# Kernel tuning notes

Measured on AMD Instinct MI355X. Metric: run time of the kernel, lower is better.

Reference implementation:

```python
import jax, jax.numpy as jnp
import numpy as np

N_NODES = 100000
N_EDGES = 640000
D_IN = 128
HIDDEN = 256
OUT = 256
NUM_GRAPHS = 256


def setup_inputs() -> dict:
    key = jax.random.key(0)
    ks = jax.random.split(key, 8)
    x = jax.random.normal(ks[0], (N_NODES, D_IN), dtype=jnp.float32)
    edge_index = jax.random.randint(ks[1], (2, N_EDGES), 0, N_NODES, dtype=jnp.int64)
    batch = jnp.sort(jax.random.randint(ks[2], (N_NODES,), 0, NUM_GRAPHS, dtype=jnp.int64))
    s1 = 1.0 / np.sqrt(D_IN)
    s2 = 1.0 / np.sqrt(HIDDEN)
    W1_l = jax.random.normal(ks[3], (D_IN, HIDDEN), dtype=jnp.float32) * s1
    W1_r = jax.random.normal(ks[4], (D_IN, HIDDEN), dtype=jnp.float32) * s1
    b1 = jnp.zeros((HIDDEN,), dtype=jnp.float32)
    W2_l = jax.random.normal(ks[5], (HIDDEN, OUT), dtype=jnp.float32) * s2
    W2_r = jax.random.normal(ks[6], (HIDDEN, OUT), dtype=jnp.float32) * s2
    b2 = jnp.zeros((OUT,), dtype=jnp.float32)
    return {"x": x, "edge_index": edge_index, "batch": batch,
            "W1_l": W1_l, "b1": b1, "W1_r": W1_r,
            "W2_l": W2_l, "b2": b2, "W2_r": W2_r}


def _sage_conv(x, src, dst, W_l, b_l, W_r):
    # PyG SAGEConv, aggr='mean': lin_l(mean_{j in N(i)} x_j) + lin_r(x_i)
    n = x.shape[0]
    msgs = x[src]                                              # [E, d] gather
    agg = jax.ops.segment_sum(msgs, dst, num_segments=n)       # [N, d] scatter-add
    cnt = jax.ops.segment_sum(jnp.ones((src.shape[0],), x.dtype), dst, num_segments=n)
    mean = agg / jnp.maximum(cnt, 1.0)[:, None]
    return mean @ W_l + b_l + x @ W_r


def reference(x, edge_index, batch, W1_l, b1, W1_r, W2_l, b2, W2_r):
    src, dst = edge_index[0], edge_index[1]
    h = jax.nn.relu(_sage_conv(x, src, dst, W1_l, b1, W1_r))
    h = _sage_conv(h, src, dst, W2_l, b2, W2_r)
    # global_add_pool: segment sum over per-node graph ids
    return jax.ops.segment_sum(h, batch, num_segments=NUM_GRAPHS)  # [G, OUT]
```

## Files before the change

kernel.cpp:

```cpp
#include <hip/hip_runtime.h>

#define NN 100000
#define NE 640000
#define DIN 128
#define DH 256
#define DOUT 256
#define NG 256
#define NB1 ((NN + 255) / 256)

#define PECH 157
#define CPE (4 * PECH)
#define PEB ((NE + CPE - 1) / CPE)
#define GSP 8

#define PNB 1024
#define CHN2 ((NN + PNB - 1) / PNB)

#define BCH 4096
#define BNB ((NE + BCH - 1) / BCH)

#define XCB (NN * DIN / 8 / 256)
#define CTB ((NE + 255) / 256)

typedef __bf16 bf16_t;
typedef __bf16 bf16x8 __attribute__((ext_vector_type(8)));
typedef __bf16 bf16x2 __attribute__((ext_vector_type(2)));
typedef float f32x4 __attribute__((ext_vector_type(4)));
typedef float f32v2 __attribute__((ext_vector_type(2)));

#if __has_builtin(__builtin_amdgcn_cvt_pk_fp8_f32) && __has_builtin(__builtin_amdgcn_cvt_pk_f32_fp8)
#define USE_HW_FP8 1
#else
#define USE_HW_FP8 0
#endif

#if !USE_HW_FP8
__device__ __forceinline__ unsigned f32_to_fp8_1(float f) {
  unsigned sg = (__float_as_uint(f) >> 31) << 7;
  float af = fabsf(f);
  unsigned body;
  if (af < 0.015625f) {
    body = (unsigned)(int)rintf(af * 512.0f);
  } else {
    unsigned bits = __float_as_uint(af);
    unsigned rb = bits + 0x7FFFFu + ((bits >> 20) & 1u);
    unsigned e = rb >> 23;
    body = ((e - 120u) << 3) | ((rb >> 20) & 7u);
  }
  return (sg | body) & 0xffu;
}
__device__ __forceinline__ float fp8_to_f32_1(unsigned b) {
  unsigned s = b >> 7, e = (b >> 3) & 15u, m = b & 7u;
  float v = (e == 0) ? (float)m * 0.001953125f
                     : __uint_as_float(((e + 120u) << 23) | (m << 20));
  return s ? -v : v;
}
#endif

__device__ __forceinline__ unsigned pack4_fp8(float v0, float v1, float v2, float v3) {
#if USE_HW_FP8
  int u = __builtin_amdgcn_cvt_pk_fp8_f32(v0, v1, 0, false);
  u = __builtin_amdgcn_cvt_pk_fp8_f32(v2, v3, u, true);
  return (unsigned)u;
#else
  return f32_to_fp8_1(v0) | (f32_to_fp8_1(v1) << 8) |
         (f32_to_fp8_1(v2) << 16) | (f32_to_fp8_1(v3) << 24);
#endif
}

__device__ __forceinline__ unsigned short pack2_fp8(float v0, float v1) {
#if USE_HW_FP8
  int u = __builtin_amdgcn_cvt_pk_fp8_f32(v0, v1, 0, false);
  return (unsigned short)(u & 0xffff);
#else
  return (unsigned short)(f32_to_fp8_1(v0) | (f32_to_fp8_1(v1) << 8));
#endif
}

__device__ __forceinline__ void unpack4_fp8(unsigned v, float* o) {
#if USE_HW_FP8
  f32v2 a = __builtin_amdgcn_cvt_pk_f32_fp8((int)v, false);
  f32v2 b = __builtin_amdgcn_cvt_pk_f32_fp8((int)v, true);
  o[0] = a[0]; o[1] = a[1]; o[2] = b[0]; o[3] = b[1];
#else
  o[0] = fp8_to_f32_1(v & 0xffu);         o[1] = fp8_to_f32_1((v >> 8) & 0xffu);
  o[2] = fp8_to_f32_1((v >> 16) & 0xffu); o[3] = fp8_to_f32_1(v >> 24);
#endif
}

__device__ __forceinline__ void unpack2_fp8(unsigned v, float* o) {
#if USE_HW_FP8
  f32v2 a = __builtin_amdgcn_cvt_pk_f32_fp8((int)v, false);
  o[0] = a[0]; o[1] = a[1];
#else
  o[0] = fp8_to_f32_1(v & 0xffu); o[1] = fp8_to_f32_1((v >> 8) & 0xffu);
#endif
}

__device__ __forceinline__ unsigned pack8_i4(const float* f) {
  unsigned nib = 0;
#pragma unroll
  for (int j = 0; j < 8; ++j) {
    int q = (int)rintf(f[j] * 2.0f);
    q = (q < -8) ? -8 : (q > 7 ? 7 : q);
    nib |= ((unsigned)(q & 15)) << (4 * j);
  }
  return nib;
}

__global__ void k_pre(const float* __restrict__ x, const int* __restrict__ dst,
                      const float* __restrict__ Wl, const float* __restrict__ Wr,
                      unsigned char* __restrict__ xf8, unsigned char* __restrict__ xi4,
                      int* __restrict__ cnt, bf16_t* __restrict__ Bp) {
  int b = blockIdx.x;
  if (b < XCB) {
    size_t i = ((size_t)b * 256 + threadIdx.x) * 8;
    float4 a = *(const float4*)(x + i), c = *(const float4*)(x + i + 4);
    uint2 p;
    p.x = pack4_fp8(a.x, a.y, a.z, a.w);
    p.y = pack4_fp8(c.x, c.y, c.z, c.w);
    *(uint2*)(xf8 + i) = p;
    float f[8] = {a.x, a.y, a.z, a.w, c.x, c.y, c.z, c.w};
    *(unsigned*)(xi4 + i / 2) = pack8_i4(f);
  } else if (b < XCB + CTB) {
    int e = (b - XCB) * 256 + threadIdx.x;
    if (e < NE) atomicAdd(&cnt[dst[e]], 1);
  } else {
    int t = (b - XCB - CTB) * 256 + threadIdx.x;
    if (t < 8192) {
      int lane = t & 63, nt = (t >> 6) & 15, kc = t >> 10;
      int n = nt * 16 + (lane & 15);
      int k0 = kc * 32 + (lane >> 4) * 8;
      bf16_t* o = Bp + ((size_t)(kc * 16 + nt) * 64 + lane) * 8;
      for (int j = 0; j < 8; ++j) {
        int k = k0 + j;
        float v = (k < 128) ? Wl[k * 256 + n] : Wr[(k - 128) * 256 + n];
        o[j] = (bf16_t)v;
      }
    }
  }
}

__global__ void k_scan1(const int* __restrict__ cnt, int* __restrict__ rpl,
                        int* __restrict__ part) {
  __shared__ int s[256];
  int t = threadIdx.x, i = blockIdx.x * 256 + t;
  int v = (i < NN) ? cnt[i] : 0;
  s[t] = v; __syncthreads();
#pragma unroll
  for (int off = 1; off < 256; off <<= 1) {
    int u = (t >= off) ? s[t - off] : 0;
    __syncthreads();
    s[t] += u;
    __syncthreads();
  }
  if (i < NN) rpl[i] = s[t] - v;
  if (t == 255) part[blockIdx.x] = s[255];
}

__global__ void k_scan2(int* __restrict__ part) {
  __shared__ int s[512];
  int t = threadIdx.x;
  int v = (t < NB1) ? part[t] : 0;
  s[t] = v; __syncthreads();
#pragma unroll
  for (int off = 1; off < 512; off <<= 1) {
    int u = (t >= off) ? s[t - off] : 0;
    __syncthreads();
    s[t] += u;
    __syncthreads();
  }
  if (t < NB1) part[t] = s[t] - v;
}

__global__ void k_finish(const int* __restrict__ rpl, const int* __restrict__ part,
                         const int* __restrict__ batch, int* __restrict__ rowptr,
                         int* __restrict__ gstart, unsigned* __restrict__ wg) {
  int n = blockIdx.x * 256 + threadIdx.x;
  if (n >= NN) return;
  int r0 = rpl[n] + part[n >> 8];
  int r1 = (n + 1 < NN) ? (rpl[n + 1] + part[(n + 1) >> 8]) : NE;
  rowptr[n] = r0;
  if (n == 0) rowptr[NN] = NE;
  int b = batch[n];
  int prev = (n == 0) ? -1 : batch[n - 1];
  for (int g = prev + 1; g <= b; ++g) gstart[g] = n;
  if (n == NN - 1) {
    for (int g = b + 1; g <= NG; ++g) gstart[g] = NN;
  }
  unsigned val = ((unsigned)b << 16) | (unsigned)(r1 - r0);
  for (int e = r0; e < r1; ++e) wg[e] = val;
}

__global__ void k_bucket(const int* __restrict__ src, const int* __restrict__ dst,
                         const int* __restrict__ rowptr, int* __restrict__ fill,
                         int* __restrict__ col) {
  int cls = blockIdx.x & 7;
  int cb = blockIdx.x >> 3;
  int e0 = cb * BCH;
  int e1 = (e0 + BCH < NE) ? e0 + BCH : NE;
  for (int e = e0 + threadIdx.x; e < e1; e += 256) {
    int d = dst[e];
    if (((d >> 4) & 7) == cls) {
      int p = rowptr[d] + atomicAdd(&fill[d], 1);
      col[p] = src[e];
    }
  }
}

__launch_bounds__(512, 4)
__global__ void k_gemm1(const unsigned char* __restrict__ xf8,
                        const unsigned char* __restrict__ xi4,
                        const int* __restrict__ rowptr, const int* __restrict__ col,
                        const float* __restrict__ b1,
                        const bf16_t* __restrict__ Bp, unsigned char* __restrict__ hf8) {
  __shared__ unsigned char smem[64 * 512];
  int n0 = blockIdx.x * 64;
  int tid = threadIdx.x;
  int wave = tid >> 6, lane = tid & 63;
  {
    int base = __builtin_amdgcn_readfirstlane(n0 + wave * 8);
    int nb1 = base + 8; if (nb1 > NN) nb1 = NN;
    if (base < NN) {
      int e = rowptr[base];
      int eTot = rowptr[nb1];
      int n = base;
      int estart = e;
      int eend = rowptr[n + 1];
      int ia0 = 0, ia1 = 0;
#define GFLUSH()                                                               \
      do {                                                                     \
        float r_ = (eend > estart)                                             \
                     ? __builtin_amdgcn_rcpf((float)(eend - estart)) : 0.f;    \
        float h_ = 0.5f * r_;                                                  \
        int row_ = n - n0;                                                     \
        unsigned sw_ = (row_ & 7) << 4;                                        \
        bf16x2 mv_;                                                            \
        mv_[0] = (bf16_t)((float)ia0 * h_); mv_[1] = (bf16_t)((float)ia1 * h_);\
        *(bf16x2*)(smem + row_ * 512 + (((unsigned)(lane * 4)) ^ sw_)) = mv_;  \
        ia0 = 0; ia1 = 0;                                                      \
        estart = eend; ++n;                                                    \
        if (n < nb1) eend = rowptr[n + 1];                                     \
      } while (0)
      while (e + 8 <= eTot) {
        unsigned v[8];
#pragma unroll
        for (int i = 0; i < 8; ++i) {
          int s = col[e + i];
          v[i] = *(const unsigned char*)(xi4 + (size_t)s * 64 + lane);
        }
#pragma unroll
        for (int i = 0; i < 8; ++i) {
          while (e + i >= eend) GFLUSH();
          int b_ = (int)v[i];
          ia0 += (b_ << 28) >> 28;
          ia1 += (b_ << 24) >> 28;
        }
        e += 8;
      }
      while (e < eTot) {
        int s = col[e];
        int b_ = (int)*(const unsigned char*)(xi4 + (size_t)s * 64 + lane);
        while (e >= eend) GFLUSH();
        ia0 += (b_ << 28) >> 28;
        ia1 += (b_ << 24) >> 28;
        ++e;
      }
      while (n < nb1) GFLUSH();
#undef GFLUSH
    }
#pragma unroll
    for (int i = 0; i < 8; ++i) {
      int node = base + i;
      int row = wave * 8 + i;
      unsigned sw = (row & 7) << 4;
      unsigned v = 0;
      if (node < NN) v = *(const unsigned short*)(xf8 + (size_t)node * DIN + lane * 2);
      float o[2]; unpack2_fp8(v, o);
      bf16x2 xv; xv[0] = (bf16_t)o[0]; xv[1] = (bf16_t)o[1];
      *(bf16x2*)(smem + row * 512 + ((unsigned)(256 + lane * 4) ^ sw)) = xv;
    }
  }
  __syncthreads();
  int lhi = lane >> 4, llo = lane & 15;
  f32x4 acc[4][2] = {};
  const bf16x8* bptr = (const bf16x8*)Bp;
#pragma unroll
  for (int kc = 0; kc < 8; ++kc) {
    bf16x8 a[4], b[2];
#pragma unroll
    for (int mi = 0; mi < 4; ++mi) {
      int row = mi * 16 + llo;
      unsigned cb = ((unsigned)((kc * 32 + lhi * 8) * 2)) ^ ((row & 7) << 4);
      a[mi] = *(const bf16x8*)(smem + row * 512 + cb);
    }
#pragma unroll
    for (int ni = 0; ni < 2; ++ni)
      b[ni] = bptr[(kc * 16 + wave * 2 + ni) * 64 + lane];
#pragma unroll
    for (int mi = 0; mi < 4; ++mi)
#pragma unroll
      for (int ni = 0; ni < 2; ++ni)
        acc[mi][ni] = __builtin_amdgcn_mfma_f32_16x16x32_bf16(a[mi], b[ni], acc[mi][ni], 0, 0, 0);
  }
  float bias[2];
#pragma unroll
  for (int ni = 0; ni < 2; ++ni) bias[ni] = b1[wave * 32 + ni * 16 + llo];
#pragma unroll
  for (int mi = 0; mi < 4; ++mi)
#pragma unroll
    for (int j = 0; j < 4; ++j) {
      int node = n0 + mi * 16 + lhi * 4 + j;
      if (node < NN) {
        float v0 = fmaxf(acc[mi][0][j] + bias[0], 0.f);
        float v1 = fmaxf(acc[mi][1][j] + bias[1], 0.f);
        unsigned short u = pack2_fp8(v0, v1);
        *(unsigned short*)(hf8 + (size_t)node * 256 + (wave >> 1) * 64 +
                           llo * 4 + (wave & 1) * 2) = u;
      }
    }
}

__global__ void k_pool(const int* __restrict__ col, const unsigned* __restrict__ wg,
                       const int* __restrict__ batch, const unsigned char* __restrict__ hf8,
                       float* __restrict__ Y1, float* __restrict__ Y2) {
  __shared__ float gbuf[GSP][256];
  int tid = threadIdx.x;
  int wv = tid >> 6, lane = tid & 63;
  int dmb = ((lane >> 4) << 6) | (lane & 15);
  float acc[4] = {0.f, 0.f, 0.f, 0.f};
  int curg = -1;
  if (blockIdx.x < PEB) {
    int c0 = blockIdx.x * CPE;
    int c1 = (c0 + CPE < NE) ? c0 + CPE : NE;
    if (c0 >= c1) return;
    int gmin = (int)(wg[c0] >> 16), gmax = (int)(wg[c1 - 1] >> 16);
    bool ldsok = (gmax - gmin) < GSP;
    for (int i = tid; i < GSP * 256; i += 256) (&gbuf[0][0])[i] = 0.f;
    __syncthreads();
    int e0 = __builtin_amdgcn_readfirstlane(c0 + wv * PECH);
    int e1 = e0 + PECH; if (e1 > c1) e1 = c1;
#define EFLUSH() do { if (curg >= 0) {                                        \
    if (ldsok) { float* gp = gbuf[curg - gmin];                               \
      atomicAdd(gp + (dmb | 0),  acc[0]); atomicAdd(gp + (dmb | 16), acc[1]); \
      atomicAdd(gp + (dmb | 32), acc[2]); atomicAdd(gp + (dmb | 48), acc[3]); \
    } else { float* yp = Y1 + (size_t)curg * 256;                             \
      unsafeAtomicAdd(yp + (dmb | 0),  acc[0]);                               \
      unsafeAtomicAdd(yp + (dmb | 16), acc[1]);                               \
      unsafeAtomicAdd(yp + (dmb | 32), acc[2]);                               \
      unsafeAtomicAdd(yp + (dmb | 48), acc[3]); }                             \
    acc[0] = acc[1] = acc[2] = acc[3] = 0.f; } } while (0)
    if (e0 < e1) {
      int e = e0;
      for (; e + 16 <= e1; e += 16) {
        unsigned wvv[16]; unsigned hv[16];
#pragma unroll
        for (int i = 0; i < 16; ++i) {
          int c = col[e + i];
          wvv[i] = wg[e + i];
          hv[i] = *(const unsigned*)(hf8 + (size_t)c * 256 + lane * 4);
        }
#pragma unroll
        for (int i = 0; i < 16; ++i) {
          int g = (int)(wvv[i] >> 16);
          if (g != curg) { EFLUSH(); curg = g; }
          float w = __builtin_amdgcn_rcpf((float)(wvv[i] & 0xffffu));
          float o[4]; unpack4_fp8(hv[i], o);
          acc[0] += w * o[0]; acc[1] += w * o[1];
          acc[2] += w * o[2]; acc[3] += w * o[3];
        }
      }
      for (; e < e1; ++e) {
        int c = col[e]; unsigned wv2 = wg[e];
        unsigned hvv = *(const unsigned*)(hf8 + (size_t)c * 256 + lane * 4);
        int g = (int)(wv2 >> 16);
        if (g != curg) { EFLUSH(); curg = g; }
        float w = __builtin_amdgcn_rcpf((float)(wv2 & 0xffffu));
        float o[4]; unpack4_fp8(hvv, o);
        acc[0] += w * o[0]; acc[1] += w * o[1];
        acc[2] += w * o[2]; acc[3] += w * o[3];
      }
      EFLUSH();
    }
#undef EFLUSH
    __syncthreads();
    if (ldsok) {
      int ng = gmax - gmin + 1;
      for (int gi = 0; gi < ng; ++gi)
        unsafeAtomicAdd(&Y1[(size_t)(gmin + gi) * 256 + tid], gbuf[gi][tid]);
    }
  } else {
    int nb = blockIdx.x - PEB;
    int n0 = nb * CHN2;
    int n1 = (n0 + CHN2 < NN) ? n0 + CHN2 : NN;
    if (n0 >= n1) return;
    int gmin = batch[n0], gmax = batch[n1 - 1];
    bool ldsok = (gmax - gmin) < GSP;
    for (int i = tid; i < GSP * 256; i += 256) (&gbuf[0][0])[i] = 0.f;
    __syncthreads();
    const int per = (CHN2 + 3) >> 2;
    int a0 = n0 + wv * per;
    int a1 = a0 + per; if (a1 > n1) a1 = n1;
#define NFLUSH() do { if (curg >= 0) {                                        \
    if (ldsok) { float* gp = gbuf[curg - gmin];                               \
      atomicAdd(gp + (dmb | 0),  acc[0]); atomicAdd(gp + (dmb | 16), acc[1]); \
      atomicAdd(gp + (dmb | 32), acc[2]); atomicAdd(gp + (dmb | 48), acc[3]); \
    } else { float* yp = Y2 + (size_t)curg * 256;                             \
      unsafeAtomicAdd(yp + (dmb | 0),  acc[0]);                               \
      unsafeAtomicAdd(yp + (dmb | 16), acc[1]);                               \
      unsafeAtomicAdd(yp + (dmb | 32), acc[2]);                               \
      unsafeAtomicAdd(yp + (dmb | 48), acc[3]); }                             \
    acc[0] = acc[1] = acc[2] = acc[3] = 0.f; } } while (0)
    for (int n = a0; n < a1; ++n) {
      int g = batch[n];
      if (g != curg) { NFLUSH(); curg = g; }
      unsigned v = *(const unsigned*)(hf8 + (size_t)n * 256 + lane * 4);
      float o[4]; unpack4_fp8(v, o);
      acc[0] += o[0]; acc[1] += o[1]; acc[2] += o[2]; acc[3] += o[3];
    }
    NFLUSH();
#undef NFLUSH
    __syncthreads();
    if (ldsok) {
      int ng = gmax - gmin + 1;
      for (int gi = 0; gi < ng; ++gi)
        unsafeAtomicAdd(&Y2[(size_t)(gmin + gi) * 256 + tid], gbuf[gi][tid]);
    }
  }
}

__global__ void k_out2(const float* __restrict__ Y1, const float* __restrict__ Y2,
                       const float* __restrict__ W2l, const float* __restrict__ W2r,
                       const float* __restrict__ b2, const int* __restrict__ gstart,
                       float* __restrict__ out) {
  __shared__ float ys[128];
  int g = blockIdx.x, ks = blockIdx.y, t = threadIdx.x;
  const float* Ysrc = (ks < 2) ? Y1 : Y2;
  const float* Wsrc = (ks < 2) ? W2l : W2r;
  int kbase = (ks & 1) * 128;
  if (t < 128) ys[t] = Ysrc[(size_t)g * 256 + kbase + t];
  __syncthreads();
  float s = 0.f;
  const float* wp = Wsrc + (size_t)kbase * 256 + t;
#pragma unroll 8
  for (int k = 0; k < 128; ++k) s += ys[k] * wp[(size_t)k * 256];
  if (ks == 0) {
    float cntf = (float)(gstart[g + 1] - gstart[g]);
    s += b2[t] * cntf;
  }
  unsafeAtomicAdd(&out[(size_t)g * 256 + t], s);
}

extern "C" void kernel_launch(void* const* d_in, const int* in_sizes, int n_in,
                              void* d_out, int out_size, void* d_ws, size_t ws_size,
                              hipStream_t stream) {
  const float* x   = (const float*)d_in[0];
  const int*   ei  = (const int*)d_in[1];
  const int*   bat = (const int*)d_in[2];
  const float* W1l = (const float*)d_in[3];
  const float* b1  = (const float*)d_in[4];
  const float* W1r = (const float*)d_in[5];
  const float* W2l = (const float*)d_in[6];
  const float* b2  = (const float*)d_in[7];
  const float* W2r = (const float*)d_in[8];
  const int* src = ei;
  const int* dst = ei + NE;

  char* ws = (char*)d_ws;
  size_t off = 0;
  int* cnt     = (int*)(ws + off); off += ((size_t)NN * 4 + 255) & ~(size_t)255;
  int* fill    = (int*)(ws + off); off += ((size_t)NN * 4 + 255) & ~(size_t)255;
  size_t zlen  = off;
  int* rpl     = (int*)(ws + off); off += ((size_t)(NN + 1) * 4 + 255) & ~(size_t)255;
  int* rowptr  = (int*)(ws + off); off += ((size_t)(NN + 1) * 4 + 255) & ~(size_t)255;
  int* part    = (int*)(ws + off); off += 512 * 4;
  int* gstart  = (int*)(ws + off); off += ((size_t)(NG + 1) * 4 + 255) & ~(size_t)255;
  int* col     = (int*)(ws + off); off += (size_t)NE * 4;
  unsigned* wg = (unsigned*)(ws + off); off += (size_t)NE * 4;
  bf16_t* Bp1  = (bf16_t*)(ws + off); off += (size_t)256 * 256 * 2;
  float* Y1    = (float*)(ws + off); off += (size_t)NG * 256 * 4;
  float* Y2    = (float*)(ws + off); off += (size_t)NG * 256 * 4;
  unsigned char* xf8 = (unsigned char*)(ws + off); off += (size_t)NN * DIN;
  unsigned char* xi4 = (unsigned char*)(ws + off); off += (size_t)NN * DIN / 2;
  unsigned char* hf8 = (unsigned char*)(ws + off); off += (size_t)NN * DH;

  hipMemsetAsync(cnt, 0, zlen, stream);
  hipMemsetAsync(Y1, 0, (size_t)NG * 256 * 4 * 2, stream);
  hipMemsetAsync(d_out, 0, (size_t)out_size * 4, stream);
  k_pre<<<XCB + CTB + 32, 256, 0, stream>>>(x, dst, W1l, W1r, xf8, xi4, cnt, Bp1);
  k_scan1<<<NB1, 256, 0, stream>>>(cnt, rpl, part);
  k_scan2<<<1, 512, 0, stream>>>(part);
  k_finish<<<NB1, 256, 0, stream>>>(rpl, part, bat, rowptr, gstart, wg);
  k_bucket<<<BNB * 8, 256, 0, stream>>>(src, dst, rowptr, fill, col);
  k_gemm1<<<(NN + 63) / 64, 512, 0, stream>>>(xf8, xi4, rowptr, col, b1, Bp1, hf8);
  k_pool<<<PEB + PNB, 256, 0, stream>>>(col, wg, bat, hf8, Y1, Y2);
  k_out2<<<dim3(NG, 4), 256, 0, stream>>>(Y1, Y2, W2l, W2r, b2, gstart, (float*)d_out);
}
```

Measured before the change: 182.8 us.

## Fuse node-sum pooling of h into gemm1 epilogue and unroll gather by 16

The per-graph sum of layer-1 activations (Y2) now accumulates in the gemm1 epilogue from the fp32 ReLU values, using an LDS graph buffer that reuses the A-tile shared memory. This removes the separate node-pool blocks in k_pool, which reread hf8. The gemm1 gather loop also gains a 16-wide unrolled stage to raise memory-level parallelism. In exchange the epilogue takes extra barriers, LDS atomics and global atomics. Y2 is now summed from unquantized values rather than fp8, a small numeric difference.

```diff
diff --git a/kernel.cpp b/kernel.cpp
--- a/kernel.cpp
+++ b/kernel.cpp
@@ -12,9 +12,6 @@
 #define CPE (4 * PECH)
 #define PEB ((NE + CPE - 1) / CPE)
 #define GSP 8
-
-#define PNB 1024
-#define CHN2 ((NN + PNB - 1) / PNB)
 
 #define BCH 4096
 #define BNB ((NE + BCH - 1) / BCH)
@@ -212,12 +209,19 @@
 __global__ void k_gemm1(const unsigned char* __restrict__ xf8,
                         const unsigned char* __restrict__ xi4,
                         const int* __restrict__ rowptr, const int* __restrict__ col,
+                        const int* __restrict__ batch,
                         const float* __restrict__ b1,
-                        const bf16_t* __restrict__ Bp, unsigned char* __restrict__ hf8) {
+                        const bf16_t* __restrict__ Bp, unsigned char* __restrict__ hf8,
+                        float* __restrict__ Y2) {
   __shared__ unsigned char smem[64 * 512];
+  __shared__ int sbatch[64];
   int n0 = blockIdx.x * 64;
   int tid = threadIdx.x;
   int wave = tid >> 6, lane = tid & 63;
+  if (tid < 64) {
+    int nn = n0 + tid;
+    sbatch[tid] = batch[(nn < NN) ? nn : (NN - 1)];
+  }
   {
     int base = __builtin_amdgcn_readfirstlane(n0 + wave * 8);
     int nb1 = base + 8; if (nb1 > NN) nb1 = NN;
@@ -242,6 +246,22 @@
         estart = eend; ++n;                                                    \
         if (n < nb1) eend = rowptr[n + 1];                                     \
       } while (0)
+      while (e + 16 <= eTot) {
+        unsigned v[16];
+#pragma unroll
+        for (int i = 0; i < 16; ++i) {
+          int s = col[e + i];
+          v[i] = *(const unsigned char*)(xi4 + (size_t)s * 64 + lane);
+        }
+#pragma unroll
+        for (int i = 0; i < 16; ++i) {
+          while (e + i >= eend) GFLUSH();
+          int b_ = (int)v[i];
+          ia0 += (b_ << 28) >> 28;
+          ia1 += (b_ << 24) >> 28;
+        }
+        e += 16;
+      }
       while (e + 8 <= eTot) {
         unsigned v[8];
 #pragma unroll
@@ -303,43 +323,73 @@
       for (int ni = 0; ni < 2; ++ni)
         acc[mi][ni] = __builtin_amdgcn_mfma_f32_16x16x32_bf16(a[mi], b[ni], acc[mi][ni], 0, 0, 0);
   }
+  __syncthreads();
+  float* gbuf2 = (float*)smem;
+  for (int i = tid; i < GSP * 256; i += 512) gbuf2[i] = 0.f;
+  __syncthreads();
+  int gmin = sbatch[0];
+  bool ldsok2 = (sbatch[63] - gmin) < GSP;
+  int d0 = wave * 32 + llo, d1 = d0 + 16;
   float bias[2];
 #pragma unroll
   for (int ni = 0; ni < 2; ++ni) bias[ni] = b1[wave * 32 + ni * 16 + llo];
+  float ya0 = 0.f, ya1 = 0.f; int yg = -1;
+#define YFLUSH() do { if (yg >= 0) {                                          \
+    if (ldsok2) {                                                             \
+      atomicAdd(&gbuf2[(yg - gmin) * 256 + d0], ya0);                         \
+      atomicAdd(&gbuf2[(yg - gmin) * 256 + d1], ya1);                         \
+    } else {                                                                  \
+      unsafeAtomicAdd(&Y2[(size_t)yg * 256 + d0], ya0);                       \
+      unsafeAtomicAdd(&Y2[(size_t)yg * 256 + d1], ya1);                       \
+    }                                                                         \
+    ya0 = 0.f; ya1 = 0.f; } } while (0)
 #pragma unroll
   for (int mi = 0; mi < 4; ++mi)
 #pragma unroll
     for (int j = 0; j < 4; ++j) {
-      int node = n0 + mi * 16 + lhi * 4 + j;
+      int lrow = mi * 16 + lhi * 4 + j;
+      int node = n0 + lrow;
       if (node < NN) {
         float v0 = fmaxf(acc[mi][0][j] + bias[0], 0.f);
         float v1 = fmaxf(acc[mi][1][j] + bias[1], 0.f);
         unsigned short u = pack2_fp8(v0, v1);
         *(unsigned short*)(hf8 + (size_t)node * 256 + (wave >> 1) * 64 +
                            llo * 4 + (wave & 1) * 2) = u;
-      }
-    }
+        int g = sbatch[lrow];
+        if (g != yg) { YFLUSH(); yg = g; }
+        ya0 += v0; ya1 += v1;
+      }
+    }
+  YFLUSH();
+#undef YFLUSH
+  __syncthreads();
+  if (ldsok2) {
+    int gspan = sbatch[63] - gmin + 1;
+    for (int i = tid; i < gspan * 256; i += 512) {
+      float v = gbuf2[i];
+      if (v != 0.f)
+        unsafeAtomicAdd(&Y2[(size_t)(gmin + (i >> 8)) * 256 + (i & 255)], v);
+    }
+  }
 }
 
 __global__ void k_pool(const int* __restrict__ col, const unsigned* __restrict__ wg,
-                       const int* __restrict__ batch, const unsigned char* __restrict__ hf8,
-                       float* __restrict__ Y1, float* __restrict__ Y2) {
+                       const unsigned char* __restrict__ hf8, float* __restrict__ Y1) {
   __shared__ float gbuf[GSP][256];
   int tid = threadIdx.x;
   int wv = tid >> 6, lane = tid & 63;
   int dmb = ((lane >> 4) << 6) | (lane & 15);
   float acc[4] = {0.f, 0.f, 0.f, 0.f};
   int curg = -1;
-  if (blockIdx.x < PEB) {
-    int c0 = blockIdx.x * CPE;
-    int c1 = (c0 + CPE < NE) ? c0 + CPE : NE;
-    if (c0 >= c1) return;
-    int gmin = (int)(wg[c0] >> 16), gmax = (int)(wg[c1 - 1] >> 16);
-    bool ldsok = (gmax - gmin) < GSP;
-    for (int i = tid; i < GSP * 256; i += 256) (&gbuf[0][0])[i] = 0.f;
-    __syncthreads();
-    int e0 = __builtin_amdgcn_readfirstlane(c0 + wv * PECH);
-    int e1 = e0 + PECH; if (e1 > c1) e1 = c1;
+  int c0 = blockIdx.x * CPE;
+  int c1 = (c0 + CPE < NE) ? c0 + CPE : NE;
+  if (c0 >= c1) return;
+  int gmin = (int)(wg[c0] >> 16), gmax = (int)(wg[c1 - 1] >> 16);
+  bool ldsok = (gmax - gmin) < GSP;
+  for (int i = tid; i < GSP * 256; i += 256) (&gbuf[0][0])[i] = 0.f;
+  __syncthreads();
+  int e0 = __builtin_amdgcn_readfirstlane(c0 + wv * PECH);
+  int e1 = e0 + PECH; if (e1 > c1) e1 = c1;
 #define EFLUSH() do { if (curg >= 0) {                                        \
     if (ldsok) { float* gp = gbuf[curg - gmin];                               \
       atomicAdd(gp + (dmb | 0),  acc[0]); atomicAdd(gp + (dmb | 16), acc[1]); \
@@ -350,82 +400,44 @@
       unsafeAtomicAdd(yp + (dmb | 32), acc[2]);                               \
       unsafeAtomicAdd(yp + (dmb | 48), acc[3]); }                             \
     acc[0] = acc[1] = acc[2] = acc[3] = 0.f; } } while (0)
-    if (e0 < e1) {
-      int e = e0;
-      for (; e + 16 <= e1; e += 16) {
-        unsigned wvv[16]; unsigned hv[16];
-#pragma unroll
-        for (int i = 0; i < 16; ++i) {
-          int c = col[e + i];
-          wvv[i] = wg[e + i];
-          hv[i] = *(const unsigned*)(hf8 + (size_t)c * 256 + lane * 4);
-        }
-#pragma unroll
-        for (int i = 0; i < 16; ++i) {
-          int g = (int)(wvv[i] >> 16);
-          if (g != curg) { EFLUSH(); curg = g; }
-          float w = __builtin_amdgcn_rcpf((float)(wvv[i] & 0xffffu));
-          float o[4]; unpack4_fp8(hv[i], o);
-          acc[0] += w * o[0]; acc[1] += w * o[1];
-          acc[2] += w * o[2]; acc[3] += w * o[3];
-        }
-      }
-      for (; e < e1; ++e) {
-        int c = col[e]; unsigned wv2 = wg[e];
-        unsigned hvv = *(const unsigned*)(hf8 + (size_t)c * 256 + lane * 4);
-        int g = (int)(wv2 >> 16);
+  if (e0 < e1) {
+    int e = e0;
+    for (; e + 16 <= e1; e += 16) {
+      unsigned wvv[16]; unsigned hv[16];
+#pragma unroll
+      for (int i = 0; i < 16; ++i) {
+        int c = col[e + i];
+        wvv[i] = wg[e + i];
+        hv[i] = *(const unsigned*)(hf8 + (size_t)c * 256 + lane * 4);
+      }
+#pragma unroll
+      for (int i = 0; i < 16; ++i) {
+        int g = (int)(wvv[i] >> 16);
         if (g != curg) { EFLUSH(); curg = g; }
-        float w = __builtin_amdgcn_rcpf((float)(wv2 & 0xffffu));
-        float o[4]; unpack4_fp8(hvv, o);
+        float w = __builtin_amdgcn_rcpf((float)(wvv[i] & 0xffffu));
+        float o[4]; unpack4_fp8(hv[i], o);
         acc[0] += w * o[0]; acc[1] += w * o[1];
         acc[2] += w * o[2]; acc[3] += w * o[3];
       }
-      EFLUSH();
-    }
+    }
+    for (; e < e1; ++e) {
+      int c = col[e]; unsigned wv2 = wg[e];
+      unsigned hvv = *(const unsigned*)(hf8 + (size_t)c * 256 + lane * 4);
+      int g = (int)(wv2 >> 16);
+      if (g != curg) { EFLUSH(); curg = g; }
+      float w = __builtin_amdgcn_rcpf((float)(wv2 & 0xffffu));
+      float o[4]; unpack4_fp8(hvv, o);
+      acc[0] += w * o[0]; acc[1] += w * o[1];
+      acc[2] += w * o[2]; acc[3] += w * o[3];
+    }
+    EFLUSH();
+  }
 #undef EFLUSH
-    __syncthreads();
-    if (ldsok) {
-      int ng = gmax - gmin + 1;
-      for (int gi = 0; gi < ng; ++gi)
-        unsafeAtomicAdd(&Y1[(size_t)(gmin + gi) * 256 + tid], gbuf[gi][tid]);
-    }
-  } else {
-    int nb = blockIdx.x - PEB;
-    int n0 = nb * CHN2;
-    int n1 = (n0 + CHN2 < NN) ? n0 + CHN2 : NN;
-    if (n0 >= n1) return;
-    int gmin = batch[n0], gmax = batch[n1 - 1];
-    bool ldsok = (gmax - gmin) < GSP;
-    for (int i = tid; i < GSP * 256; i += 256) (&gbuf[0][0])[i] = 0.f;
-    __syncthreads();
-    const int per = (CHN2 + 3) >> 2;
-    int a0 = n0 + wv * per;
-    int a1 = a0 + per; if (a1 > n1) a1 = n1;
-#define NFLUSH() do { if (curg >= 0) {                                        \
-    if (ldsok) { float* gp = gbuf[curg - gmin];                               \
-      atomicAdd(gp + (dmb | 0),  acc[0]); atomicAdd(gp + (dmb | 16), acc[1]); \
-      atomicAdd(gp + (dmb | 32), acc[2]); atomicAdd(gp + (dmb | 48), acc[3]); \
-    } else { float* yp = Y2 + (size_t)curg * 256;                             \
-      unsafeAtomicAdd(yp + (dmb | 0),  acc[0]);                               \
-      unsafeAtomicAdd(yp + (dmb | 16), acc[1]);                               \
-      unsafeAtomicAdd(yp + (dmb | 32), acc[2]);                               \
-      unsafeAtomicAdd(yp + (dmb | 48), acc[3]); }                             \
-    acc[0] = acc[1] = acc[2] = acc[3] = 0.f; } } while (0)
-    for (int n = a0; n < a1; ++n) {
-      int g = batch[n];
-      if (g != curg) { NFLUSH(); curg = g; }
-      unsigned v = *(const unsigned*)(hf8 + (size_t)n * 256 + lane * 4);
-      float o[4]; unpack4_fp8(v, o);
-      acc[0] += o[0]; acc[1] += o[1]; acc[2] += o[2]; acc[3] += o[3];
-    }
-    NFLUSH();
-#undef NFLUSH
-    __syncthreads();
-    if (ldsok) {
-      int ng = gmax - gmin + 1;
-      for (int gi = 0; gi < ng; ++gi)
-        unsafeAtomicAdd(&Y2[(size_t)(gmin + gi) * 256 + tid], gbuf[gi][tid]);
-    }
+  __syncthreads();
+  if (ldsok) {
+    int ng = gmax - gmin + 1;
+    for (int gi = 0; gi < ng; ++gi)
+      unsafeAtomicAdd(&Y1[(size_t)(gmin + gi) * 256 + tid], gbuf[gi][tid]);
   }
 }
 
@@ -492,7 +504,8 @@
   k_scan2<<<1, 512, 0, stream>>>(part);
   k_finish<<<NB1, 256, 0, stream>>>(rpl, part, bat, rowptr, gstart, wg);
   k_bucket<<<BNB * 8, 256, 0, stream>>>(src, dst, rowptr, fill, col);
-  k_gemm1<<<(NN + 63) / 64, 512, 0, stream>>>(xf8, xi4, rowptr, col, b1, Bp1, hf8);
-  k_pool<<<PEB + PNB, 256, 0, stream>>>(col, wg, bat, hf8, Y1, Y2);
+  k_gemm1<<<(NN + 63) / 64, 512, 0, stream>>>(xf8, xi4, rowptr, col, bat, b1, Bp1,
+                                              hf8, Y2);
+  k_pool<<<PEB, 256, 0, stream>>>(col, wg, hf8, Y1);
   k_out2<<<dim3(NG, 4), 256, 0, stream>>>(Y1, Y2, W2l, W2r, b2, gstart, (float*)d_out);
 }
```

Measured after the change: 173.4 us. 5.2% less time.
